# Kernel tuning notes

Hardware: AMD Instinct MI355X
Metric: run time of the kernel (lower is better)

Reference implementation:

```python
import jax, jax.numpy as jnp
import numpy as np

B, N, CIN, COUT, K, L, NNZ = 4, 4096, 128, 128, 10, 50, 65536


def _spmm(idx, vals, X):
    # COO spmm: out[r] += vals * X[c]; idx: [2, nnz], X: [N, F]
    rows, cols = idx[0], idx[1]
    return jax.ops.segment_sum(vals[:, None] * X[cols], rows, num_segments=N)

_bspmm = jax.vmap(_spmm, in_axes=(0, 0, 0))  # batched over leading dim


def _hgnn_layer(phi_idx, phi_val, inv_idx, inv_val, fea, W, d):
    # original: ((phi @ diag(d)) @ phi_inv) @ (fea @ W)
    # identical math, evaluated right-to-left to stay sparse-dense only
    filt = jnp.einsum('bnc,co->bno', fea, W)            # [B,N,COUT]
    y = _bspmm(inv_idx, inv_val, filt)                  # phi_inv @ X
    y = d[None, :, None] * y                            # diag(d) @ .
    return _bspmm(phi_idx, phi_val, y)                  # phi @ .


def setup_inputs() -> dict:
    key = jax.random.key(0)
    ks = jax.random.split(key, 20)

    def coo(ki, kv):
        idx = jax.random.randint(ki, (B, 2, NNZ), 0, N, dtype=jnp.int32)
        val = jax.random.normal(kv, (B, NNZ), jnp.float32) * 0.05
        return idx, val

    phi1_idx, phi1_val = coo(ks[0], ks[1])
    phi1_inv_idx, phi1_inv_val = coo(ks[2], ks[3])
    phi2_idx, phi2_val = coo(ks[4], ks[5])
    phi2_inv_idx, phi2_inv_val = coo(ks[6], ks[7])
    fea = jax.random.normal(ks[8], (B, N, CIN), jnp.float32)
    joblst = jax.random.randint(ks[9], (B, L), 0, N, dtype=jnp.int64)

    xavier = float(np.sqrt(6.0 / (CIN + COUT)))
    W1 = jax.random.uniform(ks[10], (CIN, COUT), jnp.float32, -xavier, xavier)
    W2 = jax.random.uniform(ks[11], (CIN, COUT), jnp.float32, -xavier, xavier)
    d1 = jax.random.uniform(ks[12], (N,), jnp.float32, 0.9, 1.1)
    d2 = jax.random.uniform(ks[13], (N,), jnp.float32, 0.9, 1.1)
    s = float(1.0 / np.sqrt(N))
    W_ih = jax.random.uniform(ks[14], (N, COUT), jnp.float32, -s, s)
    W_hh = jax.random.uniform(ks[15], (N, N), jnp.float32, -s, s)
    b_ih = jax.random.uniform(ks[16], (N,), jnp.float32, -s, s)
    b_hh = jnp.zeros((N,), jnp.float32)
    sd = float(1.0 / np.sqrt(COUT))
    dense_W = jax.random.uniform(ks[17], (K, COUT), jnp.float32, -sd, sd)
    dense_b = jnp.zeros((K,), jnp.float32)
    item_emb = jax.random.normal(ks[18], (N, COUT), jnp.float32) * 0.01

    return dict(phi1_idx=phi1_idx, phi1_val=phi1_val, phi1_inv_idx=phi1_inv_idx,
                phi1_inv_val=phi1_inv_val, phi2_idx=phi2_idx, phi2_val=phi2_val,
                phi2_inv_idx=phi2_inv_idx, phi2_inv_val=phi2_inv_val,
                fea=fea, joblst=joblst, W1=W1, d1=d1, W2=W2, d2=d2,
                W_ih=W_ih, W_hh=W_hh, b_ih=b_ih, b_hh=b_hh,
                dense_W=dense_W, dense_b=dense_b, item_emb=item_emb)


def reference(phi1_idx, phi1_val, phi1_inv_idx, phi1_inv_val,
              phi2_idx, phi2_val, phi2_inv_idx, phi2_inv_val,
              fea, joblst, W1, d1, W2, d2, W_ih, W_hh, b_ih, b_hh,
              dense_W, dense_b, item_emb):
    # two hypergraph conv layers, summed
    out1 = _hgnn_layer(phi1_idx, phi1_val, phi1_inv_idx, phi1_inv_val, fea, W1, d1)
    out2 = _hgnn_layer(phi2_idx, phi2_val, phi2_inv_idx, phi2_inv_val, fea, W2, d2)
    res = out1 + out2                                   # [B,N,COUT]

    # RNN over job history embeddings (all joblst entries valid -> no -1 filter)
    xs = jnp.swapaxes(item_emb[joblst], 0, 1)           # [L,B,COUT]
    h0 = jnp.zeros((fea.shape[0], N), fea.dtype)

    def step(h, x):
        h = jnp.tanh(x @ W_ih.T + h @ W_hh.T + b_ih + b_hh)
        return h, None

    Emb, _ = jax.lax.scan(step, h0, xs)                 # last hidden: [B,N]

    res2 = jax.nn.gelu(jnp.einsum('bno,ko->bnk', res, dense_W) + dense_b,
                       approximate=False)               # [B,N,K]
    # (res3 * Emb2).permute back == res2 * gelu(Emb) broadcast over K
    return jax.nn.sigmoid(res2 * jax.nn.gelu(Emb, approximate=False)[:, :, None])
```

## Files before the change

kernel.cpp:

```cpp
#include <hip/hip_runtime.h>
#include <cstdint>
#include <cstddef>

#define NN   4096
#define LLC  50

__device__ __forceinline__ float bf2f(unsigned short u) {
    return __uint_as_float(((unsigned)u) << 16);
}
__device__ __forceinline__ unsigned short f2bf(float x) {
    unsigned b = __float_as_uint(x);
    return (unsigned short)((b + 0x7fffu + ((b >> 16) & 1u)) >> 16);
}

#if __has_builtin(__builtin_amdgcn_sdot4)
#define SDOT4(a, b, c) __builtin_amdgcn_sdot4((int)(a), (int)(b), (c), false)
#else
__device__ __forceinline__ int sdot4_sw(unsigned a, unsigned b, int c) {
    c += (int)(signed char)(a) * (int)(signed char)(b);
    c += (int)(signed char)(a >> 8) * (int)(signed char)(b >> 8);
    c += (int)(signed char)(a >> 16) * (int)(signed char)(b >> 16);
    c += (int)(signed char)(a >> 24) * (int)(signed char)(b >> 24);
    return c;
}
#define SDOT4(a, b, c) sdot4_sw((a), (b), (c))
#endif

#define DPPADD(v, ctrl, rmask) \
    ((v) + __builtin_amdgcn_update_dpp(0, (v), (ctrl), (rmask), 0xf, true))
__device__ __forceinline__ int wred64(int v) {
    v = DPPADD(v, 0x111, 0xf);
    v = DPPADD(v, 0x112, 0xf);
    v = DPPADD(v, 0x114, 0xf);
    v = DPPADD(v, 0x118, 0xf);
    v = DPPADD(v, 0x142, 0xa);
    v = DPPADD(v, 0x143, 0xc);
    return v;
}

__global__ __launch_bounds__(128) void k_filt(const float* __restrict__ fea,
                                              const float* __restrict__ W1,
                                              const float* __restrict__ W2,
                                              unsigned short* __restrict__ f1,
                                              unsigned short* __restrict__ f2) {
    __shared__ float sfea[16][128];
    int t = threadIdx.x;
    int rb = blockIdx.x * 16;
    for (int r = 0; r < 16; ++r) sfea[r][t] = fea[(size_t)(rb + r) * 128 + t];
    __syncthreads();
    float a1[16], a2[16];
#pragma unroll
    for (int r = 0; r < 16; ++r) { a1[r] = 0.f; a2[r] = 0.f; }
    for (int c = 0; c < 128; c += 4) {
        float w10 = W1[(c + 0) * 128 + t], w11 = W1[(c + 1) * 128 + t];
        float w12 = W1[(c + 2) * 128 + t], w13 = W1[(c + 3) * 128 + t];
        float w20 = W2[(c + 0) * 128 + t], w21 = W2[(c + 1) * 128 + t];
        float w22 = W2[(c + 2) * 128 + t], w23 = W2[(c + 3) * 128 + t];
#pragma unroll
        for (int r = 0; r < 16; ++r) {
            float4 f = *(const float4*)&sfea[r][c];
            a1[r] += f.x * w10 + f.y * w11 + f.z * w12 + f.w * w13;
            a2[r] += f.x * w20 + f.y * w21 + f.z * w22 + f.w * w23;
        }
    }
#pragma unroll
    for (int r = 0; r < 16; ++r) {
        f1[(size_t)(rb + r) * 128 + t] = f2bf(a1[r]);
        f2[(size_t)(rb + r) * 128 + t] = f2bf(a2[r]);
    }
}

__global__ __launch_bounds__(256) void k_hist(const int* __restrict__ i0, const int* __restrict__ i1,
                                              const int* __restrict__ i2, const int* __restrict__ i3,
                                              int* __restrict__ counts) {
    __shared__ int lc[4096];
    int t = threadIdx.x;
#pragma unroll
    for (int i = 0; i < 16; ++i) lc[t + i * 256] = 0;
    __syncthreads();
    unsigned blk = blockIdx.x;
    unsigned s = blk >> 4, ch = blk & 15;
    unsigned m = s >> 2, b = s & 3;
    const int* ip = (m == 0) ? i0 : (m == 1) ? i1 : (m == 2) ? i2 : i3;
    unsigned base = b * 131072u + ch * 4096u;
#pragma unroll
    for (int i = 0; i < 16; ++i) {
        int r = ip[base + t + i * 256];
        atomicAdd(&lc[r], 1);
    }
    __syncthreads();
    int* cs = counts + s * 4096;
#pragma unroll
    for (int i = 0; i < 16; ++i) {
        int v = lc[t + i * 256];
        if (v) atomicAdd(cs + t + i * 256, v);
    }
}

__global__ __launch_bounds__(256) void k_scan(const int* __restrict__ counts,
                                              int* __restrict__ rowptr,
                                              int* __restrict__ cursor) {
    int s = blockIdx.x, t = threadIdx.x;
    int loc[16];
    int base = t * 16;
    const int* cs = counts + s * 4096;
    int run = 0;
#pragma unroll
    for (int i = 0; i < 16; ++i) { loc[i] = run; run += cs[base + i]; }
    int total = run;
    int lane = t & 63, wv = t >> 6;
    int v = total;
#pragma unroll
    for (int d = 1; d < 64; d <<= 1) { int u = __shfl_up(v, d, 64); if (lane >= d) v += u; }
    __shared__ int wt[4];
    if (lane == 63) wt[wv] = v;
    __syncthreads();
    int pre = v - total;
    for (int i = 0; i < wv; ++i) pre += wt[i];
    int* rp = rowptr + s * 4097;
    int* cu = cursor + s * 4096;
#pragma unroll
    for (int i = 0; i < 16; ++i) { rp[base + i] = pre + loc[i]; cu[base + i] = pre + loc[i]; }
    if (t == 255) rp[4096] = pre + total;
}

__global__ __launch_bounds__(256) void k_scatter(const int* __restrict__ i0, const int* __restrict__ i1,
                                                 const int* __restrict__ i2, const int* __restrict__ i3,
                                                 const float* __restrict__ v0, const float* __restrict__ v1,
                                                 const float* __restrict__ v2, const float* __restrict__ v3,
                                                 const float* __restrict__ d1, const float* __restrict__ d2,
                                                 int* __restrict__ cursor,
                                                 unsigned* __restrict__ ep) {
    unsigned gid = blockIdx.x * 256 + threadIdx.x;
    unsigned s = gid >> 16, e = gid & 65535;
    unsigned m = s >> 2, b = s & 3;
    const int* ip = (m == 0) ? i0 : (m == 1) ? i1 : (m == 2) ? i2 : i3;
    const float* vp = (m == 0) ? v0 : (m == 1) ? v1 : (m == 2) ? v2 : v3;
    int r = ip[(size_t)b * 131072 + e];
    int c = ip[(size_t)b * 131072 + 65536 + e];
    float v = vp[(size_t)b * 65536 + e];
    if (m == 1) v *= d1[c];
    if (m == 3) v *= d2[c];
    int pos = atomicAdd(cursor + s * 4096 + r, 1);
    ep[(size_t)s * 65536 + pos] = ((unsigned)c << 16) | (unsigned)f2bf(v);
}

__global__ __launch_bounds__(256) void k_xproj(const float* __restrict__ item_emb,
                                               const int* __restrict__ joblst,
                                               const float* __restrict__ W_ih,
                                               const float* __restrict__ b_ih,
                                               const float* __restrict__ b_hh,
                                               float* __restrict__ xp) {
    __shared__ float sx[8][128];
    int t = threadIdx.x;
    int n = blockIdx.x * 256 + t;
    int p0 = blockIdx.y * 8;
#pragma unroll
    for (int i = 0; i < 4; ++i) {
        int e2 = t + i * 256;
        int rr = e2 >> 7, c = e2 & 127;
        int p = p0 + rr;
        int b = p & 3, l = p >> 2;
        int j = joblst[b * LLC + l];
        sx[rr][c] = item_emb[(size_t)j * 128 + c];
    }
    __syncthreads();
    float acc[8];
#pragma unroll
    for (int r = 0; r < 8; ++r) acc[r] = 0.f;
    const float* wn = W_ih + (size_t)n * 128;
    for (int c = 0; c < 128; c += 4) {
        float4 w = *(const float4*)(wn + c);
#pragma unroll
        for (int r = 0; r < 8; ++r) {
            float4 xr = *(const float4*)&sx[r][c];
            acc[r] += xr.x * w.x + xr.y * w.y + xr.z * w.z + xr.w * w.w;
        }
    }
    float bias = b_ih[n] + b_hh[n];
#pragma unroll
    for (int r = 0; r < 8; ++r) xp[(size_t)(p0 + r) * NN + n] = acc[r] + bias;
}

__device__ __forceinline__ void row_acc(const unsigned* __restrict__ eps, int e0, int e1,
                                        const unsigned* __restrict__ Xd, unsigned bbase,
                                        unsigned lane, float& a0, float& a1) {
    int e = e0;
    for (; e + 8 <= e1; e += 8) {
        unsigned p[8], x[8];
#pragma unroll
        for (int i = 0; i < 8; ++i) p[i] = eps[e + i];
#pragma unroll
        for (int i = 0; i < 8; ++i)
            x[i] = Xd[((size_t)(bbase + (p[i] >> 16)) << 6) + lane];
#pragma unroll
        for (int i = 0; i < 8; ++i) {
            float v = bf2f((unsigned short)p[i]);
            a0 += v * bf2f((unsigned short)x[i]);
            a1 += v * bf2f((unsigned short)(x[i] >> 16));
        }
    }
    for (; e < e1; ++e) {
        unsigned pp = eps[e];
        unsigned xw = Xd[((size_t)(bbase + (pp >> 16)) << 6) + lane];
        float v = bf2f((unsigned short)pp);
        a0 += v * bf2f((unsigned short)xw);
        a1 += v * bf2f((unsigned short)(xw >> 16));
    }
}

__global__ __launch_bounds__(256, 2) void k_mega(
        const float* __restrict__ W_hh,
        const float* __restrict__ xp,
        unsigned* __restrict__ hq,
        float* __restrict__ hfin,
        int* __restrict__ bar,
        const int* __restrict__ rowptr,
        const unsigned* __restrict__ ep,
        const unsigned short* __restrict__ filt1,
        const unsigned short* __restrict__ filt2,
        unsigned short* __restrict__ y1,
        unsigned short* __restrict__ y2,
        float* __restrict__ res) {
    __shared__ unsigned hs[4096];
    __shared__ int red[4][16];
    __shared__ unsigned char hpk[4][4][4];
    int t = threadIdx.x;
    int lane = t & 63, wv = t >> 6;
    int blk = blockIdx.x;

    if (blk >= 256) {
        int w = blk - 256;
        int c7 = w & 7;
        {
            unsigned mm = c7 & 1, b = (unsigned)c7 >> 1;
            int s = (mm ? 8 : 0) + (int)b;
            const unsigned* Xd = (const unsigned*)(mm ? filt2 : filt1);
            unsigned* Yd = (unsigned*)(mm ? y2 : y1);
            const int* rp = rowptr + s * 4097;
            const unsigned* eps = ep + (size_t)s * 65536;
            unsigned bbase = b * 4096;
            int g = w >> 3;
            int row0 = (g * 4 + wv) * 16;
            for (int rr = 0; rr < 16; ++rr) {
                int row = row0 + rr;
                float a0 = 0.f, a1 = 0.f;
                row_acc(eps, rp[row], rp[row + 1], Xd, bbase, lane, a0, a1);
                Yd[((size_t)(bbase + row) << 6) + lane] =
                    (unsigned)f2bf(a0) | ((unsigned)f2bf(a1) << 16);
            }
        }
        __syncthreads();
        if (t == 0) {
            __builtin_amdgcn_fence(__ATOMIC_RELEASE, "agent");
            __hip_atomic_fetch_add(&bar[320], 1, __ATOMIC_RELAXED,
                                   __HIP_MEMORY_SCOPE_AGENT);
            while (__hip_atomic_load(&bar[320], __ATOMIC_RELAXED,
                                     __HIP_MEMORY_SCOPE_AGENT) < 512)
                __builtin_amdgcn_s_sleep(4);
            __builtin_amdgcn_fence(__ATOMIC_ACQUIRE, "agent");
        }
        __syncthreads();
        {
            unsigned b = (unsigned)c7 >> 1;
            unsigned bbase = b * 4096;
            const int* rpA = rowptr + (4 + (int)b) * 4097;
            const int* rpB = rowptr + (12 + (int)b) * 4097;
            const unsigned* epA = ep + (size_t)(4 + b) * 65536;
            const unsigned* epB = ep + (size_t)(12 + b) * 65536;
            const unsigned* y1d = (const unsigned*)y1;
            const unsigned* y2d = (const unsigned*)y2;
            int g2 = (w >> 3) * 2 + (w & 1);
            int row0 = (g2 * 4 + wv) * 8;
            for (int rr = 0; rr < 8; ++rr) {
                int row = row0 + rr;
                float a0 = 0.f, a1 = 0.f;
                row_acc(epA, rpA[row], rpA[row + 1], y1d, bbase, lane, a0, a1);
                row_acc(epB, rpB[row], rpB[row + 1], y2d, bbase, lane, a0, a1);
                ((float2*)res)[((size_t)(bbase + row) << 6) + lane] = make_float2(a0, a1);
            }
        }
        return;
    }

    int row_base = ((blk & 7) * 32 + (blk >> 3)) * 16;
    int wrow = row_base + wv * 4;

    uint4 W[4][4];
    {
        const float* wsrc = W_hh + (size_t)wrow * 4096;
#pragma unroll
        for (int r = 0; r < 4; ++r)
#pragma unroll
            for (int k4 = 0; k4 < 4; ++k4) {
                unsigned q[4];
#pragma unroll
                for (int i = 0; i < 4; ++i) {
                    const float* p = wsrc + (size_t)r * 4096 + (lane * 16 + k4 * 4 + i) * 4;
                    float4 w = *(const float4*)p;
                    int q0 = (int)rintf(fminf(fmaxf(w.x * 8192.f, -127.f), 127.f));
                    int q1 = (int)rintf(fminf(fmaxf(w.y * 8192.f, -127.f), 127.f));
                    int q2 = (int)rintf(fminf(fmaxf(w.z * 8192.f, -127.f), 127.f));
                    int q3 = (int)rintf(fminf(fmaxf(w.w * 8192.f, -127.f), 127.f));
                    q[i] = (q0 & 0xff) | ((q1 & 0xff) << 8) | ((q2 & 0xff) << 16) | ((q3 & 0xff) << 24);
                }
                W[r][k4] = make_uint4(q[0], q[1], q[2], q[3]);
            }
    }

    const float SC = 1.f / (8192.f * 127.f);

    for (int l = 0; l < LLC; ++l) {
        if (l > 0) {
            const unsigned* src = hq + (size_t)((l - 1) & 1) * 4096;
            unsigned sval[16];
#pragma unroll
            for (int k = 0; k < 16; ++k)
                sval[k] = __hip_atomic_load(src + t + k * 256, __ATOMIC_RELAXED,
                                            __HIP_MEMORY_SCOPE_AGENT);
#pragma unroll
            for (int k = 0; k < 16; ++k) hs[t + k * 256] = sval[k];
            __syncthreads();

            __builtin_amdgcn_s_setprio(1);
            uint4 H[4][4];
#pragma unroll
            for (int b = 0; b < 4; ++b)
#pragma unroll
                for (int k4 = 0; k4 < 4; ++k4)
                    H[b][k4] = ((const uint4*)hs)[k4 * 256 + b * 64 + lane];
            int acc[4][4];
#pragma unroll
            for (int r = 0; r < 4; ++r)
#pragma unroll
                for (int b = 0; b < 4; ++b) acc[r][b] = 0;
#pragma unroll
            for (int k4 = 0; k4 < 4; ++k4)
#pragma unroll
                for (int r = 0; r < 4; ++r)
#pragma unroll
                    for (int b = 0; b < 4; ++b) {
                        acc[r][b] = SDOT4(W[r][k4].x, H[b][k4].x, acc[r][b]);
                        acc[r][b] = SDOT4(W[r][k4].y, H[b][k4].y, acc[r][b]);
                        acc[r][b] = SDOT4(W[r][k4].z, H[b][k4].z, acc[r][b]);
                        acc[r][b] = SDOT4(W[r][k4].w, H[b][k4].w, acc[r][b]);
                    }
#pragma unroll
            for (int r = 0; r < 4; ++r)
#pragma unroll
                for (int b = 0; b < 4; ++b) acc[r][b] = wred64(acc[r][b]);
            if (lane == 63) {
#pragma unroll
                for (int b = 0; b < 4; ++b) {
                    int4 q = { acc[0][b], acc[1][b], acc[2][b], acc[3][b] };
                    *(int4*)&red[wv][b * 4] = q;
                }
            }
            __builtin_amdgcn_s_setprio(0);
        }
        if (lane < 16) {
            int b = lane >> 2, rr = lane & 3;
            int row = wrow + rr;
            float a = (l > 0) ? (float)red[wv][lane] * SC : 0.f;
            float pre = a + xp[(size_t)(l * 4 + b) * NN + row];
            float hnew = tanhf(pre);
            if (l == LLC - 1) hfin[(size_t)b * NN + row] = hnew;
            int q = (int)rintf(hnew * 127.f);
            hpk[wv][b][rr] = (unsigned char)(q & 0xff);
        }
        if (l < LLC - 1) {
            if (lane < 4) {
                int b = lane;
                unsigned d = *(const unsigned*)&hpk[wv][b][0];
                int hk = (row_base >> 2) + wv;
                int phys = ((hk >> 2) & 3) * 1024 + b * 256 + (hk >> 4) * 4 + (hk & 3);
                __hip_atomic_store(hq + (size_t)(l & 1) * 4096 + phys, d,
                                   __ATOMIC_RELAXED, __HIP_MEMORY_SCOPE_AGENT);
            }
            __syncthreads();
            if (t == 0) {
                int g = blk & 7;
                int old = __hip_atomic_fetch_add(&bar[g * 32], 1, __ATOMIC_RELAXED,
                                                 __HIP_MEMORY_SCOPE_AGENT);
                if ((old & 31) == 31)
                    __hip_atomic_fetch_add(&bar[256], 1, __ATOMIC_RELAXED,
                                           __HIP_MEMORY_SCOPE_AGENT);
                int target = 8 * (l + 1);
                while (__hip_atomic_load(&bar[256], __ATOMIC_RELAXED,
                                         __HIP_MEMORY_SCOPE_AGENT) < target)
                    __builtin_amdgcn_s_sleep(2);
            }
            __syncthreads();
        }
    }
}

__global__ __launch_bounds__(256) void k_final(const float* __restrict__ res,
                                               const float* __restrict__ dW,
                                               const float* __restrict__ db,
                                               const float* __restrict__ hfin,
                                               float* __restrict__ out) {
    __shared__ float4 sres4[512];
    __shared__ float sdw[10 * 132];
    int t = threadIdx.x;
    int row0 = blockIdx.x * 16;
    {
        const float4* src = (const float4*)(res + (size_t)row0 * 128);
        sres4[t] = src[t];
        sres4[t + 256] = src[t + 256];
    }
    for (int i = t; i < 1280; i += 256) { int k = i >> 7, c = i & 127; sdw[k * 132 + c] = dW[i]; }
    __syncthreads();
    int r = t >> 4, k = t & 15;
    if (k < 10) {
        const float* rr = (const float*)sres4 + r * 128;
        const float* wk = sdw + k * 132;
        float acc = 0.f;
#pragma unroll
        for (int c = 0; c < 128; c += 4) {
            float4 a = *(const float4*)(rr + c);
            float4 w = *(const float4*)(wk + c);
            acc += a.x * w.x + a.y * w.y + a.z * w.z + a.w * w.w;
        }
        float pre = acc + db[k];
        int grow = row0 + r;
        int b = grow >> 12, n = grow & 4095;
        float e = hfin[(size_t)b * NN + n];
        float g1 = 0.5f * pre * (1.f + erff(pre * 0.70710678118f));
        float ge = 0.5f * e * (1.f + erff(e * 0.70710678118f));
        out[(size_t)grow * 10 + k] = 1.f / (1.f + __expf(-g1 * ge));
    }
}

extern "C" void kernel_launch(void* const* d_in, const int* in_sizes, int n_in,
                              void* d_out, int out_size, void* d_ws, size_t ws_size,
                              hipStream_t stream) {
    const int*   phi1_idx = (const int*)d_in[0];
    const float* phi1_val = (const float*)d_in[1];
    const int*   inv1_idx = (const int*)d_in[2];
    const float* inv1_val = (const float*)d_in[3];
    const int*   phi2_idx = (const int*)d_in[4];
    const float* phi2_val = (const float*)d_in[5];
    const int*   inv2_idx = (const int*)d_in[6];
    const float* inv2_val = (const float*)d_in[7];
    const float* fea      = (const float*)d_in[8];
    const int*   joblst   = (const int*)d_in[9];
    const float* W1       = (const float*)d_in[10];
    const float* d1       = (const float*)d_in[11];
    const float* W2       = (const float*)d_in[12];
    const float* d2       = (const float*)d_in[13];
    const float* W_ih     = (const float*)d_in[14];
    const float* W_hh     = (const float*)d_in[15];
    const float* b_ih     = (const float*)d_in[16];
    const float* b_hh     = (const float*)d_in[17];
    const float* dense_W  = (const float*)d_in[18];
    const float* dense_b  = (const float*)d_in[19];
    const float* item_emb = (const float*)d_in[20];

    float* ws = (float*)d_ws;
    unsigned short* filt1 = (unsigned short*)ws;
    unsigned short* filt2 = (unsigned short*)(ws + 1048576);
    unsigned short* y1    = (unsigned short*)(ws + 2097152);
    unsigned short* y2    = (unsigned short*)(ws + 3145728);
    float* res  = ws + 4194304;
    float* xp   = ws + 6291456;
    float* hfin = ws + 7110656;
    unsigned* hq  = (unsigned*)(ws + 7127040);
    int*   counts = (int*)(ws + 11329536);
    int*   rowptr = (int*)(ws + 11395072);
    int*   cursor = (int*)(ws + 11460624);
    unsigned* ep  = (unsigned*)(ws + 11526160);
    int*   bar    = (int*)(ws + 12574736);

    hipMemsetAsync(counts, 0, 16 * 4096 * sizeof(int), stream);
    hipMemsetAsync(bar, 0, 2048, stream);

    k_filt<<<1024, 128, 0, stream>>>(fea, W1, W2, filt1, filt2);
    k_xproj<<<dim3(16, 25), 256, 0, stream>>>(item_emb, joblst, W_ih, b_ih, b_hh, xp);

    k_hist<<<256, 256, 0, stream>>>(inv1_idx, phi1_idx, inv2_idx, phi2_idx, counts);
    k_scan<<<16, 256, 0, stream>>>(counts, rowptr, cursor);
    k_scatter<<<4096, 256, 0, stream>>>(inv1_idx, phi1_idx, inv2_idx, phi2_idx,
                                        inv1_val, phi1_val, inv2_val, phi2_val,
                                        d1, d2, cursor, ep);

    k_mega<<<768, 256, 0, stream>>>(W_hh, xp, hq, hfin, bar,
                                    rowptr, ep, filt1, filt2, y1, y2, res);

    k_final<<<1024, 256, 0, stream>>>(res, dense_W, dense_b, hfin, (float*)d_out);
}
```

Before: 522.7 us.

## Fuse dense projection and GELU into spmm blocks, flatten RNN grid barrier

The spmm worker blocks now keep their result rows in shared memory and compute the 10-wide dense projection plus GELU directly, writing a small g1 buffer instead of the full res tensor. A tiny elementwise kernel then applies the hidden-state GELU and the sigmoid. The RNN grid barrier drops the two-level counter and has every thread poll and sum the eight group counters. The xp load is also hoisted ahead of the h exchange. This removes the res round-trip and the k_final kernel, but adds more polling traffic and lengthens the spmm blocks that share the GPU with the RNN.

```diff
diff --git a/kernel.cpp b/kernel.cpp
--- a/kernel.cpp
+++ b/kernel.cpp
@@ -221,8 +221,10 @@
         const unsigned short* __restrict__ filt2,
         unsigned short* __restrict__ y1,
         unsigned short* __restrict__ y2,
-        float* __restrict__ res) {
-    __shared__ unsigned hs[4096];
+        const float* __restrict__ dW,
+        const float* __restrict__ db,
+        float* __restrict__ g1) {
+    __shared__ unsigned hs[4352];
     __shared__ int red[4][16];
     __shared__ unsigned char hpk[4][4][4];
     int t = threadIdx.x;
@@ -272,12 +274,32 @@
             const unsigned* y2d = (const unsigned*)y2;
             int g2 = (w >> 3) * 2 + (w & 1);
             int row0 = (g2 * 4 + wv) * 8;
+            float* fs = (float*)hs + wv * 1056;
             for (int rr = 0; rr < 8; ++rr) {
                 int row = row0 + rr;
                 float a0 = 0.f, a1 = 0.f;
                 row_acc(epA, rpA[row], rpA[row + 1], y1d, bbase, lane, a0, a1);
                 row_acc(epB, rpB[row], rpB[row + 1], y2d, bbase, lane, a0, a1);
-                ((float2*)res)[((size_t)(bbase + row) << 6) + lane] = make_float2(a0, a1);
+                *(float2*)(fs + rr * 132 + 2 * lane) = make_float2(a0, a1);
+            }
+#pragma unroll
+            for (int pass = 0; pass < 2; ++pass) {
+                int task = lane + pass * 64;
+                if (task < 80) {
+                    int rr = task / 10, k = task - rr * 10;
+                    const float* rrp = fs + rr * 132;
+                    const float4* wk4 = (const float4*)(dW + (size_t)k * 128);
+                    float acc = 0.f;
+#pragma unroll
+                    for (int c4 = 0; c4 < 32; ++c4) {
+                        float4 a = *(const float4*)(rrp + c4 * 4);
+                        float4 wq = wk4[c4];
+                        acc += a.x * wq.x + a.y * wq.y + a.z * wq.z + a.w * wq.w;
+                    }
+                    float pre = acc + db[k];
+                    float gg = 0.5f * pre * (1.f + erff(pre * 0.70710678118f));
+                    g1[(size_t)(bbase + row0 + rr) * 10 + k] = gg;
+                }
             }
         }
         return;
@@ -311,6 +333,10 @@
     const float SC = 1.f / (8192.f * 127.f);
 
     for (int l = 0; l < LLC; ++l) {
+        float xpv = 0.f;
+        if (lane < 16)
+            xpv = xp[(size_t)(l * 4 + (lane >> 2)) * NN + wrow + (lane & 3)];
+
         if (l > 0) {
             const unsigned* src = hq + (size_t)((l - 1) & 1) * 4096;
             unsigned sval[16];
@@ -362,7 +388,7 @@
             int b = lane >> 2, rr = lane & 3;
             int row = wrow + rr;
             float a = (l > 0) ? (float)red[wv][lane] * SC : 0.f;
-            float pre = a + xp[(size_t)(l * 4 + b) * NN + row];
+            float pre = a + xpv;
             float hnew = tanhf(pre);
             if (l == LLC - 1) hfin[(size_t)b * NN + row] = hnew;
             int q = (int)rintf(hnew * 127.f);
@@ -378,58 +404,31 @@
                                    __ATOMIC_RELAXED, __HIP_MEMORY_SCOPE_AGENT);
             }
             __syncthreads();
-            if (t == 0) {
-                int g = blk & 7;
-                int old = __hip_atomic_fetch_add(&bar[g * 32], 1, __ATOMIC_RELAXED,
-                                                 __HIP_MEMORY_SCOPE_AGENT);
-                if ((old & 31) == 31)
-                    __hip_atomic_fetch_add(&bar[256], 1, __ATOMIC_RELAXED,
-                                           __HIP_MEMORY_SCOPE_AGENT);
-                int target = 8 * (l + 1);
-                while (__hip_atomic_load(&bar[256], __ATOMIC_RELAXED,
-                                         __HIP_MEMORY_SCOPE_AGENT) < target)
-                    __builtin_amdgcn_s_sleep(2);
-            }
-            __syncthreads();
-        }
-    }
-}
-
-__global__ __launch_bounds__(256) void k_final(const float* __restrict__ res,
-                                               const float* __restrict__ dW,
-                                               const float* __restrict__ db,
-                                               const float* __restrict__ hfin,
-                                               float* __restrict__ out) {
-    __shared__ float4 sres4[512];
-    __shared__ float sdw[10 * 132];
-    int t = threadIdx.x;
-    int row0 = blockIdx.x * 16;
-    {
-        const float4* src = (const float4*)(res + (size_t)row0 * 128);
-        sres4[t] = src[t];
-        sres4[t + 256] = src[t + 256];
-    }
-    for (int i = t; i < 1280; i += 256) { int k = i >> 7, c = i & 127; sdw[k * 132 + c] = dW[i]; }
-    __syncthreads();
-    int r = t >> 4, k = t & 15;
-    if (k < 10) {
-        const float* rr = (const float*)sres4 + r * 128;
-        const float* wk = sdw + k * 132;
-        float acc = 0.f;
-#pragma unroll
-        for (int c = 0; c < 128; c += 4) {
-            float4 a = *(const float4*)(rr + c);
-            float4 w = *(const float4*)(wk + c);
-            acc += a.x * w.x + a.y * w.y + a.z * w.z + a.w * w.w;
-        }
-        float pre = acc + db[k];
-        int grow = row0 + r;
-        int b = grow >> 12, n = grow & 4095;
-        float e = hfin[(size_t)b * NN + n];
-        float g1 = 0.5f * pre * (1.f + erff(pre * 0.70710678118f));
-        float ge = 0.5f * e * (1.f + erff(e * 0.70710678118f));
-        out[(size_t)grow * 10 + k] = 1.f / (1.f + __expf(-g1 * ge));
-    }
+            if (t == 0)
+                __hip_atomic_fetch_add(&bar[(blk & 7) * 32], 1, __ATOMIC_RELAXED,
+                                       __HIP_MEMORY_SCOPE_AGENT);
+            int target = 256 * (l + 1);
+            for (;;) {
+                int sum = 0;
+#pragma unroll
+                for (int g = 0; g < 8; ++g)
+                    sum += __hip_atomic_load(&bar[g * 32], __ATOMIC_RELAXED,
+                                             __HIP_MEMORY_SCOPE_AGENT);
+                if (sum >= target) break;
+                __builtin_amdgcn_s_sleep(2);
+            }
+        }
+    }
+}
+
+__global__ __launch_bounds__(256) void k_out(const float* __restrict__ g1,
+                                             const float* __restrict__ hfin,
+                                             float* __restrict__ out) {
+    int i = blockIdx.x * 256 + threadIdx.x;
+    int grow = i / 10;
+    float e = hfin[grow];
+    float ge = 0.5f * e * (1.f + erff(e * 0.70710678118f));
+    out[i] = 1.f / (1.f + __expf(-g1[i] * ge));
 }
 
 extern "C" void kernel_launch(void* const* d_in, const int* in_sizes, int n_in,
@@ -462,7 +461,7 @@
     unsigned short* filt2 = (unsigned short*)(ws + 1048576);
     unsigned short* y1    = (unsigned short*)(ws + 2097152);
     unsigned short* y2    = (unsigned short*)(ws + 3145728);
-    float* res  = ws + 4194304;
+    float* g1   = ws + 4194304;
     float* xp   = ws + 6291456;
     float* hfin = ws + 7110656;
     unsigned* hq  = (unsigned*)(ws + 7127040);
@@ -485,7 +484,8 @@
                                         d1, d2, cursor, ep);
 
     k_mega<<<768, 256, 0, stream>>>(W_hh, xp, hq, hfin, bar,
-                                    rowptr, ep, filt1, filt2, y1, y2, res);
-
-    k_final<<<1024, 256, 0, stream>>>(res, dense_W, dense_b, hfin, (float*)d_out);
-}
+                                    rowptr, ep, filt1, filt2, y1, y2,
+                                    dense_W, dense_b, g1);
+
+    k_out<<<640, 256, 0, stream>>>(g1, hfin, (float*)d_out);
+}
```

Result: slower. 591.2 us (+13.1%).
